# Optimization experiments

Measured on AMD Instinct MI355X. Metric: run time of the kernel, lower is better.

## Reference

```python
import jax, jax.numpy as jnp
import numpy as np

N_BINS = 15
N_SAMPLES = 2_000_000
N_CLASSES = 128


def setup_inputs() -> dict:
    key = jax.random.key(0)
    k1, k2 = jax.random.split(key)
    probs = jax.random.normal(k1, (N_SAMPLES, N_CLASSES), dtype=jnp.float32)
    labels = jax.random.randint(k2, (N_SAMPLES,), 0, N_CLASSES, dtype=jnp.int64 if jax.config.read('jax_enable_x64') else jnp.int32)
    return {"probs": probs, "labels": labels, "is_logit": 1}


def reference(probs, labels, is_logit):
    if is_logit:
        probs = jax.nn.softmax(probs, axis=-1)
    # confidences / predictions / accuracies
    confidences = jnp.max(probs, axis=1)                      # [N]
    predictions = jnp.argmax(probs, axis=1)                   # [N]
    accuracies = (predictions == labels).astype(probs.dtype)  # [N]

    # bin index for half-open bins (lower, upper]: conf in ((i)/B, (i+1)/B]
    # ceil(conf * B) - 1 maps conf==upper to bin i; clip handles conf<=0 edge.
    bin_idx = jnp.clip(jnp.ceil(confidences * N_BINS).astype(jnp.int32) - 1, 0, N_BINS - 1)

    counts = jax.ops.segment_sum(jnp.ones_like(confidences), bin_idx, num_segments=N_BINS)
    conf_sum = jax.ops.segment_sum(confidences, bin_idx, num_segments=N_BINS)
    acc_sum = jax.ops.segment_sum(accuracies, bin_idx, num_segments=N_BINS)

    n = confidences.shape[0]
    safe = jnp.maximum(counts, 1.0)
    gap = jnp.abs(conf_sum / safe - acc_sum / safe)           # [N_BINS]
    prop = counts / n                                         # [N_BINS]
    ece = jnp.sum(jnp.where(counts > 0, gap * prop, 0.0))
    return ece.reshape(1)
```

## Files before the change

kernel.cpp:

```cpp
#include <hip/hip_runtime.h>

#define N_BINS 15
#define BLOCKS 1024

typedef float f4 __attribute__((ext_vector_type(4)));

__device__ __forceinline__ float max4(f4 v) {
    return fmaxf(fmaxf(v[0], v[1]), fmaxf(v[2], v[3]));
}

__global__ __launch_bounds__(256) void ece_main(
    const float* __restrict__ probs,
    const int* __restrict__ labels,
    const int* __restrict__ is_logit_p,
    float* __restrict__ bins,
    int n_rows)
{
    __shared__ float s_bins[4][3][17];

    const int tid = threadIdx.x;
    if (tid < 4 * 3 * 17) ((float*)s_bins)[tid] = 0.f;
    __syncthreads();

    const int is_logit = *is_logit_p;
    const int lane = tid & 63;
    const int wave = tid >> 6;
    const int sub  = tid & 7;
    const int grp  = tid >> 3;

    long long row = (long long)blockIdx.x * 32 + grp;
    const long long stride = (long long)gridDim.x * 32;
    const size_t pstep = (size_t)stride * 32;

    const f4* rp = (const f4*)probs + (size_t)row * 32 + sub;

    f4 a0, a1, a2, a3;
    int lab = 0;
    bool valid = row < n_rows;
    if (valid) {
        a0 = __builtin_nontemporal_load(rp);
        a1 = __builtin_nontemporal_load(rp + 8);
        a2 = __builtin_nontemporal_load(rp + 16);
        a3 = __builtin_nontemporal_load(rp + 24);
        lab = labels[row];
    }

    while (valid) {
        const long long nrow = row + stride;
        const bool nvalid = nrow < n_rows;
        const f4* np = rp + pstep;
        f4 b0, b1, b2, b3;
        int nlab = 0;
        if (nvalid) {
            b0 = __builtin_nontemporal_load(np);
            b1 = __builtin_nontemporal_load(np + 8);
            b2 = __builtin_nontemporal_load(np + 16);
            b3 = __builtin_nontemporal_load(np + 24);
            nlab = labels[nrow];
        }

        float m = fmaxf(fmaxf(max4(a0), max4(a1)), fmaxf(max4(a2), max4(a3)));
        m = fmaxf(m, __shfl_xor(m, 1, 64));
        m = fmaxf(m, __shfl_xor(m, 2, 64));
        m = fmaxf(m, __shfl_xor(m, 4, 64));

        float conf;
        if (is_logit) {
            float e0 = (__expf(a0[0] - m) + __expf(a0[1] - m))
                     + (__expf(a0[2] - m) + __expf(a0[3] - m));
            float e1 = (__expf(a1[0] - m) + __expf(a1[1] - m))
                     + (__expf(a1[2] - m) + __expf(a1[3] - m));
            float e2 = (__expf(a2[0] - m) + __expf(a2[1] - m))
                     + (__expf(a2[2] - m) + __expf(a2[3] - m));
            float e3 = (__expf(a3[0] - m) + __expf(a3[1] - m))
                     + (__expf(a3[2] - m) + __expf(a3[3] - m));
            float s = (e0 + e1) + (e2 + e3);
            s += __shfl_xor(s, 1, 64);
            s += __shfl_xor(s, 2, 64);
            s += __shfl_xor(s, 4, 64);
            conf = 1.0f / s;
        } else {
            conf = m;
        }

        const int f = lab >> 2;
        const int c = lab & 3;
        const int k = f >> 3;
        f4 vk = (k == 0) ? a0 : (k == 1) ? a1 : (k == 2) ? a2 : a3;
        float lv = (c == 0) ? vk[0] : (c == 1) ? vk[1] : (c == 2) ? vk[2] : vk[3];
        const bool mine = ((f & 7) == sub) && (lv == m);
        const unsigned long long bal = __ballot(mine);

        if (sub == 0) {
            int bin = (int)ceilf(conf * (float)N_BINS) - 1;
            bin = bin < 0 ? 0 : (bin > N_BINS - 1 ? N_BINS - 1 : bin);
            const float acc = ((bal >> (lane & 56)) & 0xFFull) ? 1.0f : 0.0f;
            atomicAdd(&s_bins[wave][0][bin], 1.0f);
            atomicAdd(&s_bins[wave][1][bin], conf);
            atomicAdd(&s_bins[wave][2][bin], acc);
        }

        row = nrow; valid = nvalid; rp = np;
        a0 = b0; a1 = b1; a2 = b2; a3 = b3; lab = nlab;
    }

    __syncthreads();
    if (tid < 3 * N_BINS) {
        const int c = tid / N_BINS;
        const int b = tid - c * N_BINS;
        atomicAdd(&bins[tid], s_bins[0][c][b] + s_bins[1][c][b]
                            + s_bins[2][c][b] + s_bins[3][c][b]);
    }
}

__global__ void ece_final(const float* __restrict__ bins,
                          float* __restrict__ out, int n_rows)
{
    if (threadIdx.x == 0 && blockIdx.x == 0) {
        float ece = 0.f;
        for (int i = 0; i < N_BINS; ++i) {
            float c = bins[i];
            if (c > 0.f) {
                float gap = fabsf(bins[N_BINS + i] / c - bins[2 * N_BINS + i] / c);
                ece += gap * (c / (float)n_rows);
            }
        }
        out[0] = ece;
    }
}

extern "C" void kernel_launch(void* const* d_in, const int* in_sizes, int n_in,
                              void* d_out, int out_size, void* d_ws, size_t ws_size,
                              hipStream_t stream) {
    const float* probs    = (const float*)d_in[0];
    const int*   labels   = (const int*)d_in[1];
    const int*   is_logit = (const int*)d_in[2];
    float*       out      = (float*)d_out;
    float*       bins     = (float*)d_ws;
    const int n_rows = in_sizes[1];

    hipMemsetAsync(bins, 0, 3 * N_BINS * sizeof(float), stream);
    ece_main<<<BLOCKS, 256, 0, stream>>>(probs, labels, is_logit, bins, n_rows);
    ece_final<<<1, 64, 0, stream>>>(bins, out, n_rows);
}
```

Before: 1.236 ms.

## Split ECE into per-row pass and separate binning pass via workspace

Replaces the single fused kernel with two kernels. A row pass maps 32 lanes to each row, loads 8 rows per wave with fully coalesced vector loads, and writes each row's confidence and accuracy to a workspace buffer. A bin pass then histograms those values with shared-memory atomics. The aim is to decouple the atomic binning from the bandwidth-bound softmax pass, at the cost of an extra 16 MB write and read and one more kernel launch. The old fused kernel remains as a fallback, with its software prefetch removed.

```diff
diff --git a/kernel.cpp b/kernel.cpp
--- a/kernel.cpp
+++ b/kernel.cpp
@@ -1,15 +1,115 @@
 #include <hip/hip_runtime.h>
 
 #define N_BINS 15
-#define BLOCKS 1024
+#define A_BLOCKS 2048
+#define B_BLOCKS 256
 
 typedef float f4 __attribute__((ext_vector_type(4)));
+typedef float f2 __attribute__((ext_vector_type(2)));
 
 __device__ __forceinline__ float max4(f4 v) {
     return fmaxf(fmaxf(v[0], v[1]), fmaxf(v[2], v[3]));
 }
 
-__global__ __launch_bounds__(256) void ece_main(
+__global__ __launch_bounds__(256) void ece_rowpass(
+    const float* __restrict__ probs,
+    const int* __restrict__ labels,
+    const int* __restrict__ is_logit_p,
+    f2* __restrict__ rowout,
+    int n_rows)
+{
+    const int is_logit = *is_logit_p;
+    const int tid  = threadIdx.x;
+    const int lane = tid & 63;
+    const int wid  = tid >> 6;
+    const int half = lane >> 5;
+    const int col4 = lane & 31;
+
+    const long long nr = n_rows;
+    long long base = ((long long)blockIdx.x * 4 + wid) * 8;
+    const long long bstride = (long long)gridDim.x * 32;
+
+    const f4* __restrict__ pf4 = (const f4*)probs;
+
+    for (; base < nr; base += bstride) {
+        const long long cb = (base + 8 <= nr) ? base : (nr - 8);
+        const f4* p = pf4 + cb * 32 + lane;
+        const f4 v0 = __builtin_nontemporal_load(p);
+        const f4 v1 = __builtin_nontemporal_load(p + 64);
+        const f4 v2 = __builtin_nontemporal_load(p + 128);
+        const f4 v3 = __builtin_nontemporal_load(p + 192);
+
+#pragma unroll
+        for (int t = 0; t < 4; ++t) {
+            const f4 v = (t == 0) ? v0 : (t == 1) ? v1 : (t == 2) ? v2 : v3;
+            const long long r = cb + 2 * t + half;
+
+            float m = max4(v);
+            m = fmaxf(m, __shfl_xor(m, 1, 64));
+            m = fmaxf(m, __shfl_xor(m, 2, 64));
+            m = fmaxf(m, __shfl_xor(m, 4, 64));
+            m = fmaxf(m, __shfl_xor(m, 8, 64));
+            m = fmaxf(m, __shfl_xor(m, 16, 64));
+
+            float conf;
+            if (is_logit) {
+                float s = (__expf(v[0] - m) + __expf(v[1] - m))
+                        + (__expf(v[2] - m) + __expf(v[3] - m));
+                s += __shfl_xor(s, 1, 64);
+                s += __shfl_xor(s, 2, 64);
+                s += __shfl_xor(s, 4, 64);
+                s += __shfl_xor(s, 8, 64);
+                s += __shfl_xor(s, 16, 64);
+                conf = 1.0f / s;
+            } else {
+                conf = m;
+            }
+
+            const int L = labels[r];
+            const int c = L & 3;
+            const float lv = (c == 0) ? v[0] : (c == 1) ? v[1]
+                           : (c == 2) ? v[2] : v[3];
+            const bool mine = (col4 == (L >> 2)) && (lv == m);
+            const unsigned long long bal = __ballot(mine);
+            const unsigned int hbits = half ? (unsigned int)(bal >> 32)
+                                            : (unsigned int)bal;
+            if (col4 == 0) {
+                f2 o; o[0] = conf; o[1] = hbits ? 1.0f : 0.0f;
+                rowout[r] = o;
+            }
+        }
+    }
+}
+
+__global__ __launch_bounds__(256) void ece_binpass(
+    const f2* __restrict__ rowout, float* __restrict__ bins, int n_rows)
+{
+    __shared__ float s_bins[4][3][17];
+    const int tid = threadIdx.x;
+    if (tid < 4 * 3 * 17) ((float*)s_bins)[tid] = 0.f;
+    __syncthreads();
+
+    const int wave = tid >> 6;
+    for (long long i = (long long)blockIdx.x * 256 + tid; i < n_rows;
+         i += (long long)gridDim.x * 256) {
+        const f2 ca = rowout[i];
+        int bin = (int)ceilf(ca[0] * (float)N_BINS) - 1;
+        bin = bin < 0 ? 0 : (bin > N_BINS - 1 ? N_BINS - 1 : bin);
+        atomicAdd(&s_bins[wave][0][bin], 1.0f);
+        atomicAdd(&s_bins[wave][1][bin], ca[0]);
+        atomicAdd(&s_bins[wave][2][bin], ca[1]);
+    }
+
+    __syncthreads();
+    if (tid < 3 * N_BINS) {
+        const int c = tid / N_BINS;
+        const int b = tid - c * N_BINS;
+        atomicAdd(&bins[tid], s_bins[0][c][b] + s_bins[1][c][b]
+                            + s_bins[2][c][b] + s_bins[3][c][b]);
+    }
+}
+
+__global__ __launch_bounds__(256) void ece_fused(
     const float* __restrict__ probs,
     const int* __restrict__ labels,
     const int* __restrict__ is_logit_p,
@@ -17,7 +117,6 @@
     int n_rows)
 {
     __shared__ float s_bins[4][3][17];
-
     const int tid = threadIdx.x;
     if (tid < 4 * 3 * 17) ((float*)s_bins)[tid] = 0.f;
     __syncthreads();
@@ -30,51 +129,23 @@
 
     long long row = (long long)blockIdx.x * 32 + grp;
     const long long stride = (long long)gridDim.x * 32;
-    const size_t pstep = (size_t)stride * 32;
-
-    const f4* rp = (const f4*)probs + (size_t)row * 32 + sub;
-
-    f4 a0, a1, a2, a3;
-    int lab = 0;
-    bool valid = row < n_rows;
-    if (valid) {
-        a0 = __builtin_nontemporal_load(rp);
-        a1 = __builtin_nontemporal_load(rp + 8);
-        a2 = __builtin_nontemporal_load(rp + 16);
-        a3 = __builtin_nontemporal_load(rp + 24);
-        lab = labels[row];
-    }
-
-    while (valid) {
-        const long long nrow = row + stride;
-        const bool nvalid = nrow < n_rows;
-        const f4* np = rp + pstep;
-        f4 b0, b1, b2, b3;
-        int nlab = 0;
-        if (nvalid) {
-            b0 = __builtin_nontemporal_load(np);
-            b1 = __builtin_nontemporal_load(np + 8);
-            b2 = __builtin_nontemporal_load(np + 16);
-            b3 = __builtin_nontemporal_load(np + 24);
-            nlab = labels[nrow];
-        }
-
-        float m = fmaxf(fmaxf(max4(a0), max4(a1)), fmaxf(max4(a2), max4(a3)));
+
+    for (; row < n_rows; row += stride) {
+        const f4* rp = (const f4*)probs + (size_t)row * 32 + sub;
+        const f4 v0 = rp[0], v1 = rp[8], v2 = rp[16], v3 = rp[24];
+        const int lab = labels[row];
+
+        float m = fmaxf(fmaxf(max4(v0), max4(v1)), fmaxf(max4(v2), max4(v3)));
         m = fmaxf(m, __shfl_xor(m, 1, 64));
         m = fmaxf(m, __shfl_xor(m, 2, 64));
         m = fmaxf(m, __shfl_xor(m, 4, 64));
 
         float conf;
         if (is_logit) {
-            float e0 = (__expf(a0[0] - m) + __expf(a0[1] - m))
-                     + (__expf(a0[2] - m) + __expf(a0[3] - m));
-            float e1 = (__expf(a1[0] - m) + __expf(a1[1] - m))
-                     + (__expf(a1[2] - m) + __expf(a1[3] - m));
-            float e2 = (__expf(a2[0] - m) + __expf(a2[1] - m))
-                     + (__expf(a2[2] - m) + __expf(a2[3] - m));
-            float e3 = (__expf(a3[0] - m) + __expf(a3[1] - m))
-                     + (__expf(a3[2] - m) + __expf(a3[3] - m));
-            float s = (e0 + e1) + (e2 + e3);
+            float s = (__expf(v0[0]-m)+__expf(v0[1]-m))+(__expf(v0[2]-m)+__expf(v0[3]-m))
+                    + (__expf(v1[0]-m)+__expf(v1[1]-m))+(__expf(v1[2]-m)+__expf(v1[3]-m))
+                    + (__expf(v2[0]-m)+__expf(v2[1]-m))+(__expf(v2[2]-m)+__expf(v2[3]-m))
+                    + (__expf(v3[0]-m)+__expf(v3[1]-m))+(__expf(v3[2]-m)+__expf(v3[3]-m));
             s += __shfl_xor(s, 1, 64);
             s += __shfl_xor(s, 2, 64);
             s += __shfl_xor(s, 4, 64);
@@ -83,10 +154,8 @@
             conf = m;
         }
 
-        const int f = lab >> 2;
-        const int c = lab & 3;
-        const int k = f >> 3;
-        f4 vk = (k == 0) ? a0 : (k == 1) ? a1 : (k == 2) ? a2 : a3;
+        const int f = lab >> 2, c = lab & 3, k = f >> 3;
+        f4 vk = (k == 0) ? v0 : (k == 1) ? v1 : (k == 2) ? v2 : v3;
         float lv = (c == 0) ? vk[0] : (c == 1) ? vk[1] : (c == 2) ? vk[2] : vk[3];
         const bool mine = ((f & 7) == sub) && (lv == m);
         const unsigned long long bal = __ballot(mine);
@@ -99,9 +168,6 @@
             atomicAdd(&s_bins[wave][1][bin], conf);
             atomicAdd(&s_bins[wave][2][bin], acc);
         }
-
-        row = nrow; valid = nvalid; rp = np;
-        a0 = b0; a1 = b1; a2 = b2; a3 = b3; lab = nlab;
     }
 
     __syncthreads();
@@ -140,6 +206,15 @@
     const int n_rows = in_sizes[1];
 
     hipMemsetAsync(bins, 0, 3 * N_BINS * sizeof(float), stream);
-    ece_main<<<BLOCKS, 256, 0, stream>>>(probs, labels, is_logit, bins, n_rows);
+
+    const size_t need = 1024 + (size_t)n_rows * sizeof(f2);
+    if (ws_size >= need && n_rows >= 8) {
+        f2* rowout = (f2*)((char*)d_ws + 1024);
+        ece_rowpass<<<A_BLOCKS, 256, 0, stream>>>(probs, labels, is_logit,
+                                                  rowout, n_rows);
+        ece_binpass<<<B_BLOCKS, 256, 0, stream>>>(rowout, bins, n_rows);
+    } else {
+        ece_fused<<<1024, 256, 0, stream>>>(probs, labels, is_logit, bins, n_rows);
+    }
     ece_final<<<1, 64, 0, stream>>>(bins, out, n_rows);
 }
```

Result: slower. 1.326 ms (+7.2%).
